# Performance work log

Hardware: AMD Instinct MI355X
Metric: run time of the kernel (lower is better)

## Reference

```python
import jax, jax.numpy as jnp
import numpy as np

SEQ, BATCH, HID, OUT, NLAYERS = 2048, 16, 512, 10, 5


def setup_inputs() -> dict:
    key = jax.random.key(0)
    ks = jax.random.split(key, 5)
    scale_in = 1.0 / np.sqrt(HID)
    x = jax.random.normal(ks[0], (SEQ, BATCH, HID), dtype=jnp.float32)
    # Per-layer SRU weights: W maps input -> [x_tilde, f_gate, r_gate] (3H).
    Ws = jax.random.normal(ks[1], (NLAYERS, 3 * HID, HID), dtype=jnp.float32) * scale_in
    # Gate biases: [b_f, b_r] concatenated (2H per layer).
    bs = jax.random.normal(ks[2], (NLAYERS, 2 * HID), dtype=jnp.float32) * 0.1
    fc_W = jax.random.normal(ks[3], (OUT, HID), dtype=jnp.float32) * scale_in
    fc_b = jax.random.normal(ks[4], (OUT,), dtype=jnp.float32) * 0.1
    return {"x": x, "Ws": Ws, "bs": bs, "fc_W": fc_W, "fc_b": fc_b}


def _sru_layer(x, W, b):
    # x: [L, B, H]; W: [3H, H]; b: [2H]
    U = jnp.einsum("lbh,gh->lbg", x, W)  # [L, B, 3H]
    xt, zf, zr = jnp.split(U, 3, axis=-1)
    bf, br = jnp.split(b, 2)
    f = jax.nn.sigmoid(zf + bf)  # forget gate [L, B, H]
    r = jax.nn.sigmoid(zr + br)  # reset/highway gate

    def step(c_prev, inp):
        f_t, xt_t = inp
        c_t = f_t * c_prev + (1.0 - f_t) * xt_t
        return c_t, c_t

    c0 = jnp.zeros(x.shape[1:], dtype=x.dtype)
    _, c = jax.lax.scan(step, c0, (f, xt))  # c: [L, B, H]
    h = r * c + (1.0 - r) * x  # highway connection
    return h


def reference(x, Ws, bs, fc_W, fc_b):
    h = x
    for l in range(NLAYERS):
        h = _sru_layer(h, Ws[l], bs[l])
    out = jnp.einsum("lbh,oh->lbo", h, fc_W) + fc_b
    return out
```

## Files before the change

### kernel.cpp

```cpp
#include <hip/hip_runtime.h>
#include <hip/hip_bf16.h>

#define SEQ 2048
#define BATCH 16
#define HID 512
#define OUT_DIM 10
#define NLAYERS 5
#define M_ROWS (SEQ * BATCH)
#define N3H (3 * HID)
#define GK HID

#define CHUNK 32
#define NSEG (SEQ / CHUNK)

typedef __attribute__((ext_vector_type(8))) _Float16 f16x8;
typedef __attribute__((ext_vector_type(4))) float f32x4;
typedef __attribute__((ext_vector_type(8))) unsigned short u16x8;

__device__ __forceinline__ unsigned short f2h(float x) {
  return __builtin_bit_cast(unsigned short, (_Float16)x);
}
__device__ __forceinline__ float h2f(unsigned short v) {
  return (float)__builtin_bit_cast(_Float16, v);
}
__device__ __forceinline__ float sigm(float x) { return 1.f / (1.f + __expf(-x)); }

__global__ __launch_bounds__(256) void cvt_f32_to_f16(const float* __restrict__ in,
                                                      unsigned short* __restrict__ out) {
  size_t i = ((size_t)blockIdx.x * 256 + threadIdx.x) * 8;
  float4 a = *(const float4*)(in + i);
  float4 b = *(const float4*)(in + i + 4);
  u16x8 r;
  r[0] = f2h(a.x); r[1] = f2h(a.y); r[2] = f2h(a.z); r[3] = f2h(a.w);
  r[4] = f2h(b.x); r[5] = f2h(b.y); r[6] = f2h(b.z); r[7] = f2h(b.w);
  *(u16x8*)(out + i) = r;
}

__global__ __launch_bounds__(256) void gemm_mfma(const unsigned short* __restrict__ A,
                                                 const unsigned short* __restrict__ B,
                                                 unsigned short* __restrict__ C) {
  __shared__ unsigned short lds[3][8192];
  const int tid = threadIdx.x;
  const int nwg = (M_ROWS / 128) * (N3H / 128);
  const int cpx = nwg / 8;
  const int swz = (blockIdx.x % 8) * cpx + blockIdx.x / 8;
  const int bm = swz / (N3H / 128);
  const int bn = swz % (N3H / 128);
  const int lane = tid & 63;
  const int wid = tid >> 6;
  const int wm = (wid >> 1) * 64, wn = (wid & 1) * 64;

  const unsigned short* Ag = A + (size_t)bm * 128 * GK;
  const unsigned short* Bg = B + (size_t)bn * 128 * GK;

  const int s0 = tid, s1 = tid + 256;
  const int r0 = s0 >> 2, c0 = (s0 & 3) * 8;
  const int r1 = s1 >> 2, c1 = (s1 & 3) * 8;

  const int fr = lane & 15;
  const int ko = (lane >> 4) * 8;

  f32x4 acc[4][4];
#pragma unroll
  for (int i = 0; i < 4; ++i)
#pragma unroll
    for (int j = 0; j < 4; ++j) acc[i][j] = (f32x4){0.f, 0.f, 0.f, 0.f};

#define STAGE(buf, k0)                                                                              \
  {                                                                                                 \
    __builtin_amdgcn_global_load_lds(                                                               \
        (const __attribute__((address_space(1))) void*)(Ag + (size_t)r0 * GK + (k0) + c0),          \
        (__attribute__((address_space(3))) void*)&lds[buf][s0 * 8], 16, 0, 0);                      \
    __builtin_amdgcn_global_load_lds(                                                               \
        (const __attribute__((address_space(1))) void*)(Ag + (size_t)r1 * GK + (k0) + c1),          \
        (__attribute__((address_space(3))) void*)&lds[buf][s1 * 8], 16, 0, 0);                      \
    __builtin_amdgcn_global_load_lds(                                                               \
        (const __attribute__((address_space(1))) void*)(Bg + (size_t)r0 * GK + (k0) + c0),          \
        (__attribute__((address_space(3))) void*)&lds[buf][4096 + s0 * 8], 16, 0, 0);               \
    __builtin_amdgcn_global_load_lds(                                                               \
        (const __attribute__((address_space(1))) void*)(Bg + (size_t)r1 * GK + (k0) + c1),          \
        (__attribute__((address_space(3))) void*)&lds[buf][4096 + s1 * 8], 16, 0, 0);               \
  }

  STAGE(0, 0);
  STAGE(1, 32);
#pragma unroll 1
  for (int kt = 0; kt < 16; ++kt) {
    if (kt < 15) {
      asm volatile("s_waitcnt vmcnt(4)" ::: "memory");
    } else {
      asm volatile("s_waitcnt vmcnt(0)" ::: "memory");
    }
    __builtin_amdgcn_s_barrier();
    __builtin_amdgcn_sched_barrier(0);
    if (kt + 2 < 16) STAGE((kt + 2) % 3, (kt + 2) * 32);
    const int cb = kt % 3;
    f16x8 af[4], bfr[4];
#pragma unroll
    for (int t = 0; t < 4; ++t) {
      af[t]  = *(const f16x8*)&lds[cb][(wm + t * 16 + fr) * 32 + ko];
      bfr[t] = *(const f16x8*)&lds[cb][4096 + (wn + t * 16 + fr) * 32 + ko];
    }
#pragma unroll
    for (int mt = 0; mt < 4; ++mt)
#pragma unroll
      for (int nt = 0; nt < 4; ++nt)
        acc[mt][nt] = __builtin_amdgcn_mfma_f32_16x16x32_f16(af[mt], bfr[nt], acc[mt][nt], 0, 0, 0);
  }
#undef STAGE

  __syncthreads();
  unsigned short* cl = &lds[0][0];
  const int er = (lane >> 4) * 4;
#pragma unroll
  for (int mt = 0; mt < 4; ++mt)
#pragma unroll
    for (int nt = 0; nt < 4; ++nt) {
      const int row = wm + mt * 16 + er;
      const int col = wn + nt * 16 + fr;
#pragma unroll
      for (int j = 0; j < 4; ++j) cl[(row + j) * 136 + col] = f2h(acc[mt][nt][j]);
    }
  __syncthreads();
  unsigned short* Cb = C + (size_t)bm * 128 * N3H + bn * 128;
#pragma unroll
  for (int i = 0; i < 8; ++i) {
    int flat = i * 2048 + tid * 8;
    int r = flat >> 7, c = flat & 127;
    *(u16x8*)(Cb + (size_t)r * N3H + c) = *(const u16x8*)&cl[r * 136 + c];
  }
}

__global__ __launch_bounds__(256, 4) void sru_scan_fused(
    const unsigned short* __restrict__ U,
    const float* __restrict__ bias,
    unsigned long long* __restrict__ FC,
    unsigned short* hb) {
  const int s = blockIdx.x >> 4;
  const int b = blockIdx.x & 15;
  const int h0 = threadIdx.x << 1;
  const float bf0 = bias[h0], bf1 = bias[h0 + 1];
  const float br0 = bias[HID + h0], br1 = bias[HID + h0 + 1];

  const size_t rowstep = (size_t)BATCH * N3H;
  const unsigned short* Up = U + ((size_t)(s * CHUNK) * BATCH + b) * N3H + h0;

  unsigned fx0[CHUNK], fx1[CHUNK];
  float F0 = 1.f, F1 = 1.f, c0 = 0.f, c1 = 0.f;
#pragma unroll
  for (int i = 0; i < CHUNK; ++i) {
    const unsigned short* p = Up + (size_t)i * rowstep;
    unsigned xt = *(const unsigned*)(p);
    unsigned zf = *(const unsigned*)(p + HID);
    unsigned short fh0 = f2h(sigm(h2f((unsigned short)zf) + bf0));
    unsigned short fh1 = f2h(sigm(h2f((unsigned short)(zf >> 16)) + bf1));
    float f0 = h2f(fh0), f1 = h2f(fh1);
    c0 = f0 * c0 + (1.f - f0) * h2f((unsigned short)xt);
    c1 = f1 * c1 + (1.f - f1) * h2f((unsigned short)(xt >> 16));
    F0 *= f0; F1 *= f1;
    fx0[i] = (xt & 0xffffu) | ((unsigned)fh0 << 16);
    fx1[i] = (xt >> 16) | ((unsigned)fh1 << 16);
  }

  const size_t ch = ((size_t)s * BATCH + b) * HID + h0;
  atomicExch(&FC[ch],
             ((unsigned long long)__builtin_bit_cast(unsigned, c0) << 32) |
                 __builtin_bit_cast(unsigned, -F0));
  atomicExch(&FC[ch + 1],
             ((unsigned long long)__builtin_bit_cast(unsigned, c1) << 32) |
                 __builtin_bit_cast(unsigned, -F1));

  float ci0 = 0.f, ci1 = 0.f, P0 = 1.f, P1 = 1.f;
  for (int j = s - 1; j >= 0; --j) {
    const size_t cj = ((size_t)j * BATCH + b) * HID + h0;
    unsigned long long v0, v1;
    do { v0 = atomicAdd(&FC[cj], 0ULL); } while (!(v0 & 0x80000000ULL));
    do { v1 = atomicAdd(&FC[cj + 1], 0ULL); } while (!(v1 & 0x80000000ULL));
    float Fj0 = -__builtin_bit_cast(float, (unsigned)v0);
    float Cj0 = __builtin_bit_cast(float, (unsigned)(v0 >> 32));
    float Fj1 = -__builtin_bit_cast(float, (unsigned)v1);
    float Cj1 = __builtin_bit_cast(float, (unsigned)(v1 >> 32));
    ci0 += P0 * Cj0; P0 *= Fj0;
    ci1 += P1 * Cj1; P1 *= Fj1;
    if (P0 < 1e-5f && P1 < 1e-5f) break;
  }

  float cc0 = ci0, cc1 = ci1;
  const size_t hstep = (size_t)BATCH * HID;
  unsigned short* hp = hb + ((size_t)(s * CHUNK) * BATCH + b) * HID + h0;
#pragma unroll
  for (int i = 0; i < CHUNK; ++i) {
    unsigned zr = *(const unsigned*)(Up + (size_t)i * rowstep + 2 * HID);
    unsigned xv = *(const unsigned*)(hp + (size_t)i * hstep);
    float f0 = h2f((unsigned short)(fx0[i] >> 16));
    float f1 = h2f((unsigned short)(fx1[i] >> 16));
    cc0 = f0 * cc0 + (1.f - f0) * h2f((unsigned short)fx0[i]);
    cc1 = f1 * cc1 + (1.f - f1) * h2f((unsigned short)fx1[i]);
    float r0 = sigm(h2f((unsigned short)zr) + br0);
    float r1 = sigm(h2f((unsigned short)(zr >> 16)) + br1);
    float hn0 = r0 * cc0 + (1.f - r0) * h2f((unsigned short)xv);
    float hn1 = r1 * cc1 + (1.f - r1) * h2f((unsigned short)(xv >> 16));
    *(unsigned*)(hp + (size_t)i * hstep) = (unsigned)f2h(hn0) | ((unsigned)f2h(hn1) << 16);
  }
}

#define FCR 16
__global__ __launch_bounds__(256) void fc_kernel(const unsigned short* __restrict__ H,
                                                 const float* __restrict__ W,
                                                 const float* __restrict__ bv,
                                                 float* __restrict__ out) {
  __shared__ float hs[FCR][516];
  __shared__ float ws[OUT_DIM][516];
  const int tid = threadIdx.x;
  const size_t m0 = (size_t)blockIdx.x * FCR;
#pragma unroll
  for (int i = 0; i < 4; ++i) {
    int f = tid + i * 256;
    int row = f >> 6;
    int kq = f & 63;
    u16x8 v = *(const u16x8*)(H + (m0 + row) * 512 + kq * 8);
#pragma unroll
    for (int j = 0; j < 8; ++j) hs[row][kq * 8 + j] = h2f(v[j]);
  }
#pragma unroll
  for (int i = 0; i < 5; ++i) {
    int f = tid + i * 256;
    int row = f >> 7;
    int kq = f & 127;
    float4 v = *(const float4*)(W + row * 512 + kq * 4);
    *(float4*)&ws[row][kq * 4] = v;
  }
  __syncthreads();
  if (tid < FCR * OUT_DIM) {
    int row = tid / OUT_DIM;
    int o = tid - row * OUT_DIM;
    float acc = bv[o];
#pragma unroll 8
    for (int k = 0; k < 512; ++k) acc += hs[row][k] * ws[o][k];
    out[(m0 + row) * OUT_DIM + o] = acc;
  }
}

extern "C" void kernel_launch(void* const* d_in, const int* in_sizes, int n_in,
                              void* d_out, int out_size, void* d_ws, size_t ws_size,
                              hipStream_t stream) {
  const float* x   = (const float*)d_in[0];
  const float* Ws  = (const float*)d_in[1];
  const float* bs  = (const float*)d_in[2];
  const float* fcW = (const float*)d_in[3];
  const float* fcb = (const float*)d_in[4];
  float* out = (float*)d_out;

  char* ws = (char*)d_ws;
  const size_t MiB = 1024 * 1024;
  unsigned short* Ub = (unsigned short*)ws;
  unsigned short* hb = (unsigned short*)(ws + 96 * MiB);
  unsigned short* Wh = (unsigned short*)(ws + 128 * MiB);
  unsigned long long* FC = (unsigned long long*)(ws + 136 * MiB);

  hipMemsetAsync(FC, 0, (size_t)NLAYERS * NSEG * BATCH * HID * 8, stream);
  cvt_f32_to_f16<<<(NLAYERS * N3H * HID) / (256 * 8), 256, 0, stream>>>(Ws, Wh);
  cvt_f32_to_f16<<<(M_ROWS * HID) / (256 * 8), 256, 0, stream>>>(x, hb);

  for (int l = 0; l < NLAYERS; ++l) {
    gemm_mfma<<<(M_ROWS / 128) * (N3H / 128), 256, 0, stream>>>(
        hb, Wh + (size_t)l * N3H * HID, Ub);
    sru_scan_fused<<<NSEG * BATCH, 256, 0, stream>>>(
        Ub, bs + (size_t)l * 2 * HID,
        FC + (size_t)l * NSEG * BATCH * HID, hb);
  }
  fc_kernel<<<M_ROWS / FCR, 256, 0, stream>>>(hb, fcW, fcb, out);
}
```

Measured before the change: 612.2 us.

## Fuse gate sigmoid+bias into GEMM epilogue and vectorize scan per wave

The GEMM epilogue now adds the gate biases and applies the sigmoid for the f and r column blocks, so it stores activated gates in fp16. The scan kernel is reorganised so each wave handles one (segment, batch) pair with 8 hidden units per lane, using 16-byte vector loads instead of 32-bit loads. It also drops the register-cached fx arrays and rereads U in the second pass. This targets narrow memory accesses and per-element sigmoid work in the scan. In exchange the decoupled-lookback spin loop now waits on 8 flags per lane across fewer, wider blocks, and U is read twice.

```diff
diff --git a/kernel.cpp b/kernel.cpp
--- a/kernel.cpp
+++ b/kernel.cpp
@@ -38,6 +38,7 @@
 
 __global__ __launch_bounds__(256) void gemm_mfma(const unsigned short* __restrict__ A,
                                                  const unsigned short* __restrict__ B,
+                                                 const float* __restrict__ bias,
                                                  unsigned short* __restrict__ C) {
   __shared__ unsigned short lds[3][8192];
   const int tid = threadIdx.x;
@@ -112,14 +113,20 @@
   __syncthreads();
   unsigned short* cl = &lds[0][0];
   const int er = (lane >> 4) * 4;
+  const bool gated = (bn >= 4);
 #pragma unroll
   for (int mt = 0; mt < 4; ++mt)
 #pragma unroll
     for (int nt = 0; nt < 4; ++nt) {
       const int row = wm + mt * 16 + er;
       const int col = wn + nt * 16 + fr;
-#pragma unroll
-      for (int j = 0; j < 4; ++j) cl[(row + j) * 136 + col] = f2h(acc[mt][nt][j]);
+      const float bv = gated ? bias[bn * 128 + col - 512] : 0.f;
+#pragma unroll
+      for (int j = 0; j < 4; ++j) {
+        float v = acc[mt][nt][j];
+        if (gated) v = sigm(v + bv);
+        cl[(row + j) * 136 + col] = f2h(v);
+      }
     }
   __syncthreads();
   unsigned short* Cb = C + (size_t)bm * 128 * N3H + bn * 128;
@@ -131,76 +138,88 @@
   }
 }
 
-__global__ __launch_bounds__(256, 4) void sru_scan_fused(
+__global__ __launch_bounds__(256) void sru_scan_fused(
     const unsigned short* __restrict__ U,
-    const float* __restrict__ bias,
     unsigned long long* __restrict__ FC,
     unsigned short* hb) {
-  const int s = blockIdx.x >> 4;
-  const int b = blockIdx.x & 15;
-  const int h0 = threadIdx.x << 1;
-  const float bf0 = bias[h0], bf1 = bias[h0 + 1];
-  const float br0 = bias[HID + h0], br1 = bias[HID + h0 + 1];
+  const int wid = threadIdx.x >> 6;
+  const int lane = threadIdx.x & 63;
+  const int p = blockIdx.x * 4 + wid;
+  const int s = p >> 4;
+  const int b = p & 15;
+  const int h0 = lane * 8;
 
   const size_t rowstep = (size_t)BATCH * N3H;
   const unsigned short* Up = U + ((size_t)(s * CHUNK) * BATCH + b) * N3H + h0;
 
-  unsigned fx0[CHUNK], fx1[CHUNK];
-  float F0 = 1.f, F1 = 1.f, c0 = 0.f, c1 = 0.f;
-#pragma unroll
+  float F[8], c[8];
+#pragma unroll
+  for (int j = 0; j < 8; ++j) { F[j] = 1.f; c[j] = 0.f; }
+#pragma unroll 4
   for (int i = 0; i < CHUNK; ++i) {
-    const unsigned short* p = Up + (size_t)i * rowstep;
-    unsigned xt = *(const unsigned*)(p);
-    unsigned zf = *(const unsigned*)(p + HID);
-    unsigned short fh0 = f2h(sigm(h2f((unsigned short)zf) + bf0));
-    unsigned short fh1 = f2h(sigm(h2f((unsigned short)(zf >> 16)) + bf1));
-    float f0 = h2f(fh0), f1 = h2f(fh1);
-    c0 = f0 * c0 + (1.f - f0) * h2f((unsigned short)xt);
-    c1 = f1 * c1 + (1.f - f1) * h2f((unsigned short)(xt >> 16));
-    F0 *= f0; F1 *= f1;
-    fx0[i] = (xt & 0xffffu) | ((unsigned)fh0 << 16);
-    fx1[i] = (xt >> 16) | ((unsigned)fh1 << 16);
+    const unsigned short* up = Up + (size_t)i * rowstep;
+    u16x8 xt = *(const u16x8*)(up);
+    u16x8 fv = *(const u16x8*)(up + HID);
+#pragma unroll
+    for (int j = 0; j < 8; ++j) {
+      float f = h2f(fv[j]);
+      c[j] = f * c[j] + (1.f - f) * h2f(xt[j]);
+      F[j] *= f;
+    }
   }
 
   const size_t ch = ((size_t)s * BATCH + b) * HID + h0;
-  atomicExch(&FC[ch],
-             ((unsigned long long)__builtin_bit_cast(unsigned, c0) << 32) |
-                 __builtin_bit_cast(unsigned, -F0));
-  atomicExch(&FC[ch + 1],
-             ((unsigned long long)__builtin_bit_cast(unsigned, c1) << 32) |
-                 __builtin_bit_cast(unsigned, -F1));
-
-  float ci0 = 0.f, ci1 = 0.f, P0 = 1.f, P1 = 1.f;
-  for (int j = s - 1; j >= 0; --j) {
-    const size_t cj = ((size_t)j * BATCH + b) * HID + h0;
-    unsigned long long v0, v1;
-    do { v0 = atomicAdd(&FC[cj], 0ULL); } while (!(v0 & 0x80000000ULL));
-    do { v1 = atomicAdd(&FC[cj + 1], 0ULL); } while (!(v1 & 0x80000000ULL));
-    float Fj0 = -__builtin_bit_cast(float, (unsigned)v0);
-    float Cj0 = __builtin_bit_cast(float, (unsigned)(v0 >> 32));
-    float Fj1 = -__builtin_bit_cast(float, (unsigned)v1);
-    float Cj1 = __builtin_bit_cast(float, (unsigned)(v1 >> 32));
-    ci0 += P0 * Cj0; P0 *= Fj0;
-    ci1 += P1 * Cj1; P1 *= Fj1;
-    if (P0 < 1e-5f && P1 < 1e-5f) break;
-  }
-
-  float cc0 = ci0, cc1 = ci1;
+#pragma unroll
+  for (int j = 0; j < 8; ++j)
+    atomicExch(&FC[ch + j],
+               ((unsigned long long)__builtin_bit_cast(unsigned, c[j]) << 32) |
+                   __builtin_bit_cast(unsigned, -F[j]));
+
+  float ci[8], P[8];
+#pragma unroll
+  for (int j = 0; j < 8; ++j) { ci[j] = 0.f; P[j] = 1.f; }
+  for (int jj = s - 1; jj >= 0; --jj) {
+    const size_t cj = ((size_t)jj * BATCH + b) * HID + h0;
+    unsigned long long v[8];
+#pragma unroll
+    for (int j = 0; j < 8; ++j) v[j] = atomicAdd(&FC[cj + j], 0ULL);
+    bool all;
+    do {
+      all = true;
+#pragma unroll
+      for (int j = 0; j < 8; ++j)
+        if (!(v[j] & 0x80000000ULL)) { v[j] = atomicAdd(&FC[cj + j], 0ULL); all = false; }
+    } while (!all);
+    float pm = 0.f;
+#pragma unroll
+    for (int j = 0; j < 8; ++j) {
+      float Fj = -__builtin_bit_cast(float, (unsigned)v[j]);
+      float Cj = __builtin_bit_cast(float, (unsigned)(v[j] >> 32));
+      ci[j] += P[j] * Cj;
+      P[j] *= Fj;
+      pm = fmaxf(pm, P[j]);
+    }
+    if (pm < 1e-5f) break;
+  }
+
   const size_t hstep = (size_t)BATCH * HID;
   unsigned short* hp = hb + ((size_t)(s * CHUNK) * BATCH + b) * HID + h0;
-#pragma unroll
+#pragma unroll 4
   for (int i = 0; i < CHUNK; ++i) {
-    unsigned zr = *(const unsigned*)(Up + (size_t)i * rowstep + 2 * HID);
-    unsigned xv = *(const unsigned*)(hp + (size_t)i * hstep);
-    float f0 = h2f((unsigned short)(fx0[i] >> 16));
-    float f1 = h2f((unsigned short)(fx1[i] >> 16));
-    cc0 = f0 * cc0 + (1.f - f0) * h2f((unsigned short)fx0[i]);
-    cc1 = f1 * cc1 + (1.f - f1) * h2f((unsigned short)fx1[i]);
-    float r0 = sigm(h2f((unsigned short)zr) + br0);
-    float r1 = sigm(h2f((unsigned short)(zr >> 16)) + br1);
-    float hn0 = r0 * cc0 + (1.f - r0) * h2f((unsigned short)xv);
-    float hn1 = r1 * cc1 + (1.f - r1) * h2f((unsigned short)(xv >> 16));
-    *(unsigned*)(hp + (size_t)i * hstep) = (unsigned)f2h(hn0) | ((unsigned)f2h(hn1) << 16);
+    const unsigned short* up = Up + (size_t)i * rowstep;
+    u16x8 xt = *(const u16x8*)(up);
+    u16x8 fv = *(const u16x8*)(up + HID);
+    u16x8 rv = *(const u16x8*)(up + 2 * HID);
+    u16x8 hv = *(const u16x8*)(hp + (size_t)i * hstep);
+    u16x8 ho;
+#pragma unroll
+    for (int j = 0; j < 8; ++j) {
+      float f = h2f(fv[j]);
+      float r = h2f(rv[j]);
+      ci[j] = f * ci[j] + (1.f - f) * h2f(xt[j]);
+      ho[j] = f2h(r * ci[j] + (1.f - r) * h2f(hv[j]));
+    }
+    *(u16x8*)(hp + (size_t)i * hstep) = ho;
   }
 }
 
@@ -264,10 +283,9 @@
 
   for (int l = 0; l < NLAYERS; ++l) {
     gemm_mfma<<<(M_ROWS / 128) * (N3H / 128), 256, 0, stream>>>(
-        hb, Wh + (size_t)l * N3H * HID, Ub);
-    sru_scan_fused<<<NSEG * BATCH, 256, 0, stream>>>(
-        Ub, bs + (size_t)l * 2 * HID,
-        FC + (size_t)l * NSEG * BATCH * HID, hb);
+        hb, Wh + (size_t)l * N3H * HID, bs + (size_t)l * 2 * HID, Ub);
+    sru_scan_fused<<<NSEG * BATCH / 4, 256, 0, stream>>>(
+        Ub, FC + (size_t)l * NSEG * BATCH * HID, hb);
   }
   fc_kernel<<<M_ROWS / FCR, 256, 0, stream>>>(hb, fcW, fcb, out);
 }
```

Result: slower. 703.7 us (+14.9%).

## Replace 128x128 GEMM with 256x256 8-wave eight-phase pipelined MFMA kernel

Applied to the files above, without the earlier changes.

Replaces the per-layer 128x128-tile, 4-wave GEMM with a 256x256-tile, 8-wave kernel. The K loop is split into eight phases that interleave LDS fragment loads, async global-to-LDS prefetch with a deeper ring of buffers, barriers, and MFMA bursts under raised wave priority. The goal is more data reuse per loaded tile and better overlap of memory traffic with matrix math. In exchange it needs about 132 KB of LDS, allows one workgroup per CU, and launches only 768 workgroups, which makes occupancy and tail effects a risk.

```diff
diff --git a/kernel.cpp b/kernel.cpp
--- a/kernel.cpp
+++ b/kernel.cpp
@@ -36,98 +36,121 @@
   *(u16x8*)(out + i) = r;
 }
 
-__global__ __launch_bounds__(256) void gemm_mfma(const unsigned short* __restrict__ A,
-                                                 const unsigned short* __restrict__ B,
-                                                 unsigned short* __restrict__ C) {
-  __shared__ unsigned short lds[3][8192];
+__global__ __launch_bounds__(512, 1) void gemm_8ph(const unsigned short* __restrict__ A,
+                                                   const unsigned short* __restrict__ B,
+                                                   unsigned short* __restrict__ C) {
+  __shared__ __align__(16) unsigned short lds[67584];
   const int tid = threadIdx.x;
-  const int nwg = (M_ROWS / 128) * (N3H / 128);
+  const int nwg = (M_ROWS / 256) * (N3H / 256);
   const int cpx = nwg / 8;
   const int swz = (blockIdx.x % 8) * cpx + blockIdx.x / 8;
-  const int bm = swz / (N3H / 128);
-  const int bn = swz % (N3H / 128);
+  const int bm = swz / (N3H / 256);
+  const int bn = swz % (N3H / 256);
   const int lane = tid & 63;
   const int wid = tid >> 6;
-  const int wm = (wid >> 1) * 64, wn = (wid & 1) * 64;
-
-  const unsigned short* Ag = A + (size_t)bm * 128 * GK;
-  const unsigned short* Bg = B + (size_t)bn * 128 * GK;
-
-  const int s0 = tid, s1 = tid + 256;
-  const int r0 = s0 >> 2, c0 = (s0 & 3) * 8;
-  const int r1 = s1 >> 2, c1 = (s1 & 3) * 8;
-
+  const int wr = wid >> 2;
+  const int wc = wid & 3;
   const int fr = lane & 15;
-  const int ko = (lane >> 4) * 8;
-
-  f32x4 acc[4][4];
-#pragma unroll
-  for (int i = 0; i < 4; ++i)
+  const int koq = lane >> 4;
+
+  const unsigned short* Ag = A + (size_t)bm * 256 * GK;
+  const unsigned short* Bg = B + (size_t)bn * 256 * GK;
+
+  const int srow = wid * 32 + (lane >> 2);
+  const int sk8 = (lane & 3) * 8;
+
+#define ISSUE_STAGE(j)                                                                              \
+  if ((j) < 32) {                                                                                   \
+    const int Ts = (j) >> 2, kcs = ((j) >> 1) & 1, isB = (j) & 1;                                   \
+    const unsigned short* gsrc = isB ? Bg : Ag;                                                     \
+    const int kb = Ts * 64 + kcs * 32;                                                              \
+    const int pl = (isB ? 32768 : 0) + (((Ts & 1) * 2 + kcs) << 13);                                \
+    __builtin_amdgcn_global_load_lds(                                                               \
+        (const __attribute__((address_space(1))) void*)(gsrc + (size_t)srow * GK + kb + sk8),       \
+        (__attribute__((address_space(3))) void*)&lds[pl + wid * 1024 + lane * 8], 16, 0, 0);       \
+    __builtin_amdgcn_global_load_lds(                                                               \
+        (const __attribute__((address_space(1))) void*)(gsrc + (size_t)(srow + 16) * GK + kb + sk8),\
+        (__attribute__((address_space(3))) void*)&lds[pl + wid * 1024 + 512 + lane * 8], 16, 0, 0); \
+  }
+
+  f32x4 acc[8][4];
+#pragma unroll
+  for (int i = 0; i < 8; ++i)
 #pragma unroll
     for (int j = 0; j < 4; ++j) acc[i][j] = (f32x4){0.f, 0.f, 0.f, 0.f};
 
-#define STAGE(buf, k0)                                                                              \
+  f16x8 bfr[4];
+
+#define PHASE(p, t)                                                                                 \
   {                                                                                                 \
-    __builtin_amdgcn_global_load_lds(                                                               \
-        (const __attribute__((address_space(1))) void*)(Ag + (size_t)r0 * GK + (k0) + c0),          \
-        (__attribute__((address_space(3))) void*)&lds[buf][s0 * 8], 16, 0, 0);                      \
-    __builtin_amdgcn_global_load_lds(                                                               \
-        (const __attribute__((address_space(1))) void*)(Ag + (size_t)r1 * GK + (k0) + c1),          \
-        (__attribute__((address_space(3))) void*)&lds[buf][s1 * 8], 16, 0, 0);                      \
-    __builtin_amdgcn_global_load_lds(                                                               \
-        (const __attribute__((address_space(1))) void*)(Bg + (size_t)r0 * GK + (k0) + c0),          \
-        (__attribute__((address_space(3))) void*)&lds[buf][4096 + s0 * 8], 16, 0, 0);               \
-    __builtin_amdgcn_global_load_lds(                                                               \
-        (const __attribute__((address_space(1))) void*)(Bg + (size_t)r1 * GK + (k0) + c1),          \
-        (__attribute__((address_space(3))) void*)&lds[buf][4096 + s1 * 8], 16, 0, 0);               \
-  }
-
-  STAGE(0, 0);
-  STAGE(1, 32);
+    constexpr int par = ((p) > 4) ? 1 : 0;                                                          \
+    constexpr int kc = (((p)-1) >> 1) & 1;                                                          \
+    constexpr int mg = ((p)-1) & 1;                                                                 \
+    constexpr int apl = (par * 2 + kc) << 13;                                                       \
+    constexpr int bpl = 32768 + ((par * 2 + kc) << 13);                                             \
+    f16x8 af[4];                                                                                    \
+    _Pragma("unroll") for (int m2 = 0; m2 < 4; ++m2)                                                \
+        af[m2] = *(const f16x8*)&lds[apl + (wr * 128 + (mg * 4 + m2) * 16 + fr) * 32 + koq * 8];    \
+    if (mg == 0) {                                                                                  \
+      _Pragma("unroll") for (int n2 = 0; n2 < 4; ++n2)                                              \
+          bfr[n2] = *(const f16x8*)&lds[bpl + (wc * 64 + n2 * 16 + fr) * 32 + koq * 8];             \
+    }                                                                                               \
+    ISSUE_STAGE(8 * (t) + (p) + 5);                                                                 \
+    __builtin_amdgcn_s_barrier();                                                                   \
+    __builtin_amdgcn_sched_barrier(0);                                                              \
+    __builtin_amdgcn_s_setprio(1);                                                                  \
+    _Pragma("unroll") for (int m2 = 0; m2 < 4; ++m2)                                                \
+      _Pragma("unroll") for (int n2 = 0; n2 < 4; ++n2)                                              \
+        acc[mg * 4 + m2][n2] =                                                                      \
+            __builtin_amdgcn_mfma_f32_16x16x32_f16(af[m2], bfr[n2], acc[mg * 4 + m2][n2], 0, 0, 0); \
+    __builtin_amdgcn_s_setprio(0);                                                                  \
+    if ((p) % 2 == 0) {                                                                             \
+      if ((t) < 3) {                                                                                \
+        asm volatile("s_waitcnt vmcnt(8)" ::: "memory");                                            \
+      } else if ((p) == 2) {                                                                        \
+        asm volatile("s_waitcnt vmcnt(8)" ::: "memory");                                            \
+      } else if ((p) == 4) {                                                                        \
+        asm volatile("s_waitcnt vmcnt(4)" ::: "memory");                                            \
+      } else if ((p) == 6) {                                                                        \
+        asm volatile("s_waitcnt vmcnt(0)" ::: "memory");                                            \
+      }                                                                                             \
+    }                                                                                               \
+    __builtin_amdgcn_s_barrier();                                                                   \
+    __builtin_amdgcn_sched_barrier(0);                                                              \
+  }
+
+#pragma unroll
+  for (int js = 0; js < 6; ++js) ISSUE_STAGE(js);
+  asm volatile("s_waitcnt vmcnt(8)" ::: "memory");
+  __builtin_amdgcn_s_barrier();
+  __builtin_amdgcn_sched_barrier(0);
+
 #pragma unroll 1
-  for (int kt = 0; kt < 16; ++kt) {
-    if (kt < 15) {
-      asm volatile("s_waitcnt vmcnt(4)" ::: "memory");
-    } else {
-      asm volatile("s_waitcnt vmcnt(0)" ::: "memory");
-    }
-    __builtin_amdgcn_s_barrier();
-    __builtin_amdgcn_sched_barrier(0);
-    if (kt + 2 < 16) STAGE((kt + 2) % 3, (kt + 2) * 32);
-    const int cb = kt % 3;
-    f16x8 af[4], bfr[4];
-#pragma unroll
-    for (int t = 0; t < 4; ++t) {
-      af[t]  = *(const f16x8*)&lds[cb][(wm + t * 16 + fr) * 32 + ko];
-      bfr[t] = *(const f16x8*)&lds[cb][4096 + (wn + t * 16 + fr) * 32 + ko];
-    }
-#pragma unroll
-    for (int mt = 0; mt < 4; ++mt)
-#pragma unroll
-      for (int nt = 0; nt < 4; ++nt)
-        acc[mt][nt] = __builtin_amdgcn_mfma_f32_16x16x32_f16(af[mt], bfr[nt], acc[mt][nt], 0, 0, 0);
-  }
-#undef STAGE
+  for (int t = 0; t < 4; ++t) {
+    PHASE(1, t) PHASE(2, t) PHASE(3, t) PHASE(4, t)
+    PHASE(5, t) PHASE(6, t) PHASE(7, t) PHASE(8, t)
+  }
+#undef PHASE
+#undef ISSUE_STAGE
 
   __syncthreads();
-  unsigned short* cl = &lds[0][0];
   const int er = (lane >> 4) * 4;
 #pragma unroll
-  for (int mt = 0; mt < 4; ++mt)
-#pragma unroll
-    for (int nt = 0; nt < 4; ++nt) {
-      const int row = wm + mt * 16 + er;
-      const int col = wn + nt * 16 + fr;
-#pragma unroll
-      for (int j = 0; j < 4; ++j) cl[(row + j) * 136 + col] = f2h(acc[mt][nt][j]);
+  for (int mf = 0; mf < 8; ++mf)
+#pragma unroll
+    for (int nf = 0; nf < 4; ++nf) {
+      const int row = wr * 128 + mf * 16 + er;
+      const int col = wc * 64 + nf * 16 + fr;
+#pragma unroll
+      for (int j = 0; j < 4; ++j) lds[(row + j) * 264 + col] = f2h(acc[mf][nf][j]);
     }
   __syncthreads();
-  unsigned short* Cb = C + (size_t)bm * 128 * N3H + bn * 128;
-#pragma unroll
-  for (int i = 0; i < 8; ++i) {
-    int flat = i * 2048 + tid * 8;
-    int r = flat >> 7, c = flat & 127;
-    *(u16x8*)(Cb + (size_t)r * N3H + c) = *(const u16x8*)&cl[r * 136 + c];
+  unsigned short* Cb = C + (size_t)bm * 256 * N3H + bn * 256;
+#pragma unroll
+  for (int i = 0; i < 16; ++i) {
+    int flat = i * 4096 + tid * 8;
+    int r = flat >> 8, c = flat & 255;
+    *(u16x8*)(Cb + (size_t)r * N3H + c) = *(const u16x8*)&lds[r * 264 + c];
   }
 }
 
@@ -263,7 +286,7 @@
   cvt_f32_to_f16<<<(M_ROWS * HID) / (256 * 8), 256, 0, stream>>>(x, hb);
 
   for (int l = 0; l < NLAYERS; ++l) {
-    gemm_mfma<<<(M_ROWS / 128) * (N3H / 128), 256, 0, stream>>>(
+    gemm_8ph<<<(M_ROWS / 256) * (N3H / 256), 512, 0, stream>>>(
         hb, Wh + (size_t)l * N3H * HID, Ub);
     sru_scan_fused<<<NSEG * BATCH, 256, 0, stream>>>(
         Ub, bs + (size_t)l * 2 * HID,
```

Result: slower. 633.0 us (+3.4%).

## Rewrite final FC as wave-per-row-group kernel with register-held weights

Applied to the files above, without the earlier changes.

Replaces the shared-memory FC kernel, where only 160 of 256 threads computed and each walked the full 512-long dot product serially, with a kernel where each wave owns 32 rows. Each lane keeps an 8-wide slice of all 10 weight rows in registers and reduces partial sums with xor shuffles. This removes the shared-memory staging, the block sync and the idle threads, and uses fully coalesced reads of H. In exchange it does 10 six-step shuffle reductions per row and launches only 1024 waves, which lowers parallelism.

```diff
diff --git a/kernel.cpp b/kernel.cpp
--- a/kernel.cpp
+++ b/kernel.cpp
@@ -204,40 +204,43 @@
   }
 }
 
-#define FCR 16
-__global__ __launch_bounds__(256) void fc_kernel(const unsigned short* __restrict__ H,
-                                                 const float* __restrict__ W,
-                                                 const float* __restrict__ bv,
-                                                 float* __restrict__ out) {
-  __shared__ float hs[FCR][516];
-  __shared__ float ws[OUT_DIM][516];
-  const int tid = threadIdx.x;
-  const size_t m0 = (size_t)blockIdx.x * FCR;
-#pragma unroll
-  for (int i = 0; i < 4; ++i) {
-    int f = tid + i * 256;
-    int row = f >> 6;
-    int kq = f & 63;
-    u16x8 v = *(const u16x8*)(H + (m0 + row) * 512 + kq * 8);
-#pragma unroll
-    for (int j = 0; j < 8; ++j) hs[row][kq * 8 + j] = h2f(v[j]);
-  }
-#pragma unroll
-  for (int i = 0; i < 5; ++i) {
-    int f = tid + i * 256;
-    int row = f >> 7;
-    int kq = f & 127;
-    float4 v = *(const float4*)(W + row * 512 + kq * 4);
-    *(float4*)&ws[row][kq * 4] = v;
-  }
-  __syncthreads();
-  if (tid < FCR * OUT_DIM) {
-    int row = tid / OUT_DIM;
-    int o = tid - row * OUT_DIM;
-    float acc = bv[o];
-#pragma unroll 8
-    for (int k = 0; k < 512; ++k) acc += hs[row][k] * ws[o][k];
-    out[(m0 + row) * OUT_DIM + o] = acc;
+__global__ __launch_bounds__(256) void fc_wave(const unsigned short* __restrict__ H,
+                                               const float* __restrict__ W,
+                                               const float* __restrict__ bv,
+                                               float* __restrict__ out) {
+  const int lane = threadIdx.x & 63;
+  const int wave = blockIdx.x * 4 + (threadIdx.x >> 6);
+  const int k0 = lane * 8;
+
+  float wreg[OUT_DIM][8];
+#pragma unroll
+  for (int o = 0; o < OUT_DIM; ++o) {
+    float4 a = *(const float4*)(W + o * HID + k0);
+    float4 b = *(const float4*)(W + o * HID + k0 + 4);
+    wreg[o][0] = a.x; wreg[o][1] = a.y; wreg[o][2] = a.z; wreg[o][3] = a.w;
+    wreg[o][4] = b.x; wreg[o][5] = b.y; wreg[o][6] = b.z; wreg[o][7] = b.w;
+  }
+  const float bo = (lane < OUT_DIM) ? bv[lane] : 0.f;
+
+  const size_t row0 = (size_t)wave * 32;
+#pragma unroll 1
+  for (int i = 0; i < 32; ++i) {
+    const size_t row = row0 + i;
+    u16x8 hv8 = *(const u16x8*)(H + row * HID + k0);
+    float hv[8];
+#pragma unroll
+    for (int j = 0; j < 8; ++j) hv[j] = h2f(hv8[j]);
+    float vout = 0.f;
+#pragma unroll
+    for (int o = 0; o < OUT_DIM; ++o) {
+      float p = 0.f;
+#pragma unroll
+      for (int j = 0; j < 8; ++j) p += hv[j] * wreg[o][j];
+#pragma unroll
+      for (int m = 32; m > 0; m >>= 1) p += __shfl_xor(p, m);
+      if (lane == o) vout = p;
+    }
+    if (lane < OUT_DIM) out[row * OUT_DIM + lane] = vout + bo;
   }
 }
 
@@ -269,5 +272,5 @@
         Ub, bs + (size_t)l * 2 * HID,
         FC + (size_t)l * NSEG * BATCH * HID, hb);
   }
-  fc_kernel<<<M_ROWS / FCR, 256, 0, stream>>>(hb, fcW, fcb, out);
-}
+  fc_wave<<<256, 256, 0, stream>>>(hb, fcW, fcb, out);
+}
```

Measured after the change: 627.1 us. +2.4%, slower.
